# Kernel optimization log

Measured on AMD Instinct MI355X. Metric: run time of the kernel, lower is better.

Reference implementation:

```python
import jax, jax.numpy as jnp
import numpy as np

HEADS = 16
DIM_HEAD = 64

def setup_inputs() -> dict:
    key = jax.random.key(0)
    k1, k2, k3 = jax.random.split(key, 3)
    B, F, N, DIM = 4, 16, 196, 1024
    ntok = 1 + F * N  # cls + frames*patches
    x = jax.random.normal(k1, (B, ntok, DIM), dtype=jnp.float32)
    w_qkv = jax.random.normal(k2, (DIM, 3 * HEADS * DIM_HEAD), dtype=jnp.float32) * (DIM ** -0.5)
    w_out = jax.random.normal(k3, (HEADS * DIM_HEAD, DIM), dtype=jnp.float32) * ((HEADS * DIM_HEAD) ** -0.5)
    return {"x": x, "w_qkv": w_qkv, "w_out": w_out, "f": F}

def _attn(q, k, v):
    # q: [b, i, d], k/v: [b, j, d]
    sim = jnp.einsum('bid,bjd->bij', q, k)
    a = jax.nn.softmax(sim, axis=-1)
    return jnp.einsum('bij,bjd->bid', a, v)

def reference(x, w_qkv, w_out, f):
    B, ntok, dim = x.shape
    h, dh = HEADS, DIM_HEAD
    n = (ntok - 1) // f  # patches per frame
    scale = dh ** -0.5

    qkv = x @ w_qkv  # [B, ntok, 3*h*dh]
    q, k, v = jnp.split(qkv, 3, axis=-1)
    # 'b n (h d) -> (b h) n d'
    def split_heads(t):
        return t.reshape(B, ntok, h, dh).transpose(0, 2, 1, 3).reshape(B * h, ntok, dh)
    q, k, v = split_heads(q) * scale, split_heads(k), split_heads(v)

    cls_q, q_ = q[:, :1], q[:, 1:]
    cls_k, k_ = k[:, :1], k[:, 1:]
    cls_v, v_ = v[:, :1], v[:, 1:]

    # cls token attends to everything
    cls_out = _attn(cls_q, k, v)  # [(b h), 1, d]

    # axial rearrange: '(b h) (f n) d -> (b h f) n d' (spatial attention)
    def to_axial(t):
        return t.reshape(B * h, f, n, dh).reshape(B * h * f, n, dh)
    q_, k_, v_ = map(to_axial, (q_, k_, v_))

    # broadcast cls kv to each frame: 'b () d -> (b r) () d', r = f
    cls_k_r = jnp.repeat(cls_k, f, axis=0)
    cls_v_r = jnp.repeat(cls_v, f, axis=0)
    k_ = jnp.concatenate((cls_k_r, k_), axis=1)  # [(b h f), 1+n, d]
    v_ = jnp.concatenate((cls_v_r, v_), axis=1)

    out = _attn(q_, k_, v_)  # [(b h f), n, d]
    # back: '(b h f) n d -> (b h) (f n) d'
    out = out.reshape(B * h, f * n, dh)
    out = jnp.concatenate((cls_out, out), axis=1)  # [(b h), ntok, d]
    # '(b h) n d -> b n (h d)'
    out = out.reshape(B, h, ntok, dh).transpose(0, 2, 1, 3).reshape(B, ntok, h * dh)
    return out @ w_out
```

## Files before the change

kernel.cpp:

```cpp
#include <hip/hip_runtime.h>
#include <stdint.h>

typedef unsigned short u16;
typedef unsigned int u32;
typedef __attribute__((ext_vector_type(4))) float f32x4;
typedef __attribute__((ext_vector_type(4))) float float4v;
typedef __attribute__((ext_vector_type(8))) short short8;
typedef __attribute__((ext_vector_type(4))) u32 u32x4;
typedef __attribute__((ext_vector_type(4))) u16 u16x4;
typedef __attribute__((ext_vector_type(8))) u16 u16x8;

#define DEV static __device__ __forceinline__

#define NTOK 3137
#define MROWS 12548
#define NHEAD 16
#define DH 64
#define NKT 16

DEV float bf2f(u16 h){ u32 u = ((u32)h)<<16; float f; __builtin_memcpy(&f,&u,4); return f; }
DEV u16 f2bf(float f){ u32 u; __builtin_memcpy(&u,&f,4); u32 r = u + 0x7FFFu + ((u>>16)&1u); return (u16)(r>>16); }

DEV void gl_lds16(const u16* g, u16* l){
  __builtin_amdgcn_global_load_lds((const __attribute__((address_space(1))) void*)g,
                                   (__attribute__((address_space(3))) void*)l, 16, 0, 0);
}

#define BARRIER()  asm volatile("s_barrier" ::: "memory")
#define WAIT_LGKM0() asm volatile("s_waitcnt lgkmcnt(0)" ::: "memory")
#define WAIT_VM(n)  asm volatile("s_waitcnt vmcnt(" #n ")" ::: "memory")

__global__ __launch_bounds__(256) void cast_bf16_kernel(const float* __restrict__ in,
                                                        u16* __restrict__ out, int n4){
  int i = blockIdx.x*256 + threadIdx.x;
  int stride = gridDim.x*256;
  for(; i < n4; i += stride){
    float4v v = *(const float4v*)(in + (size_t)i*4);
    u16x4 o;
    for(int e=0;e<4;++e) o[e] = f2bf(v[e]);
    *(u16x4*)(out + (size_t)i*4) = o;
  }
}

__global__ void transpose_cast_kernel(const float* __restrict__ in, u16* __restrict__ out,
                                      int R, int C){
  __shared__ float tile[32][33];
  int c0 = blockIdx.x<<5, r0 = blockIdx.y<<5;
  int tx = threadIdx.x, ty = threadIdx.y;
  for(int k=0;k<32;k+=8) tile[ty+k][tx] = in[(size_t)(r0+ty+k)*C + c0+tx];
  __syncthreads();
  for(int k=0;k<32;k+=8) out[(size_t)(c0+ty+k)*R + r0+tx] = f2bf(tile[tx][ty+k]);
}

template<int EPI>
__global__ __launch_bounds__(512, 2) void gemm256_kernel(
    const u16* __restrict__ A, const u16* __restrict__ Bt,
    u16* __restrict__ Qb, u16* __restrict__ Kb, u16* __restrict__ Vb,
    float* __restrict__ Out, int Mtot, int tilesx)
{
  __shared__ __align__(16) char smem[131072];
  const int tid = threadIdx.x, lane = tid & 63, wid = tid >> 6;
  const int wr = wid >> 2, wc = wid & 3;

  const int nwg = gridDim.x, chunk = nwg >> 3, orig = blockIdx.x;
  const int wg = (orig & 7)*chunk + (orig >> 3);
  const int by = wg / tilesx, bx = wg - by*tilesx;
  const int m0 = by << 8, n0 = bx << 8;

  f32x4 acc[8][4];
  #pragma unroll
  for(int i=0;i<8;++i)
    #pragma unroll
    for(int j=0;j<4;++j) acc[i][j] = (f32x4){0.f,0.f,0.f,0.f};

  auto STAGE = [&](int t, int hi){
    const int bsel = t & 1;
    char* base = smem + bsel*65536 + ((hi>>1)<<15) + ((hi&1)<<14);
    const u16* mat = (hi < 2) ? A : Bt;
    const int rbase = ((hi < 2) ? m0 : n0) + ((hi&1)<<7);
    #pragma unroll
    for(int j=0;j<2;++j){
      int idx = j*512 + tid;
      int r = idx >> 3;
      int c2s = ((idx&7)<<4) ^ ((r&7)<<4);
      int grow = rbase + r;
      if(hi < 2 && grow >= Mtot) grow = Mtot - 1;
      const u16* src = mat + (size_t)grow*1024 + t*64 + (c2s>>1);
      u16* dst = (u16*)(base + j*8192 + wid*1024);
      gl_lds16(src, dst);
    }
  };

  const int rA   = (lane&15)*128;
  const int csw0 = (((lane>>4)<<4)      ) ^ ((lane&7)<<4);
  const int csw1 = (((lane>>4)<<4) + 64 ) ^ ((lane&7)<<4);

  auto RDA = [&](int bsel, int i, int kk)->short8 {
    const char* p = smem + bsel*65536 + (wr<<14) + (i<<4)*128 + rA + (kk ? csw1 : csw0);
    return *(const short8*)p;
  };
  auto RDB = [&](int bsel, int jn, int kk)->short8 {
    const char* p = smem + bsel*65536 + 32768 + ((wc>>1)<<14)
                  + (((wc&1)<<6) + (jn<<4))*128 + rA + (kk ? csw1 : csw0);
    return *(const short8*)p;
  };

  STAGE(0,0); STAGE(0,1); STAGE(0,2); STAGE(0,3); STAGE(1,0);
  WAIT_VM(2);
  BARRIER();

  short8 aR[4][2], b0[2][2], b1[2][2];
  for(int t=0; t<NKT; ++t){
    const int bs = t & 1;
    #pragma unroll
    for(int i=0;i<4;++i){ aR[i][0]=RDA(bs,i,0); aR[i][1]=RDA(bs,i,1); }
    #pragma unroll
    for(int j=0;j<2;++j){ b0[j][0]=RDB(bs,j,0); b0[j][1]=RDB(bs,j,1); }
    if(t+1<NKT) STAGE(t+1,1);
    BARRIER(); WAIT_LGKM0();
    __builtin_amdgcn_s_setprio(1);
    #pragma unroll
    for(int i=0;i<4;++i)
      #pragma unroll
      for(int j=0;j<2;++j){
        acc[i][j] = __builtin_amdgcn_mfma_f32_16x16x32_bf16(aR[i][0], b0[j][0], acc[i][j], 0,0,0);
        acc[i][j] = __builtin_amdgcn_mfma_f32_16x16x32_bf16(aR[i][1], b0[j][1], acc[i][j], 0,0,0);
      }
    __builtin_amdgcn_s_setprio(0);
    BARRIER();
    #pragma unroll
    for(int j=0;j<2;++j){ b1[j][0]=RDB(bs,2+j,0); b1[j][1]=RDB(bs,2+j,1); }
    if(t+1<NKT) STAGE(t+1,2);
    BARRIER(); WAIT_LGKM0();
    __builtin_amdgcn_s_setprio(1);
    #pragma unroll
    for(int i=0;i<4;++i)
      #pragma unroll
      for(int j=0;j<2;++j){
        acc[i][2+j] = __builtin_amdgcn_mfma_f32_16x16x32_bf16(aR[i][0], b1[j][0], acc[i][2+j], 0,0,0);
        acc[i][2+j] = __builtin_amdgcn_mfma_f32_16x16x32_bf16(aR[i][1], b1[j][1], acc[i][2+j], 0,0,0);
      }
    __builtin_amdgcn_s_setprio(0);
    BARRIER();
    #pragma unroll
    for(int i=0;i<4;++i){ aR[i][0]=RDA(bs,4+i,0); aR[i][1]=RDA(bs,4+i,1); }
    if(t+1<NKT) STAGE(t+1,3);
    BARRIER(); WAIT_LGKM0();
    __builtin_amdgcn_s_setprio(1);
    #pragma unroll
    for(int i=0;i<4;++i)
      #pragma unroll
      for(int j=0;j<2;++j){
        acc[4+i][2+j] = __builtin_amdgcn_mfma_f32_16x16x32_bf16(aR[i][0], b1[j][0], acc[4+i][2+j], 0,0,0);
        acc[4+i][2+j] = __builtin_amdgcn_mfma_f32_16x16x32_bf16(aR[i][1], b1[j][1], acc[4+i][2+j], 0,0,0);
      }
    __builtin_amdgcn_s_setprio(0);
    BARRIER();
    if(t+2<NKT) STAGE(t+2,0);
    if(t < NKT-2){ WAIT_VM(2); } else { WAIT_VM(0); }
    BARRIER();
    __builtin_amdgcn_s_setprio(1);
    #pragma unroll
    for(int i=0;i<4;++i)
      #pragma unroll
      for(int j=0;j<2;++j){
        acc[4+i][j] = __builtin_amdgcn_mfma_f32_16x16x32_bf16(aR[i][0], b0[j][0], acc[4+i][j], 0,0,0);
        acc[4+i][j] = __builtin_amdgcn_mfma_f32_16x16x32_bf16(aR[i][1], b0[j][1], acc[4+i][j], 0,0,0);
      }
    __builtin_amdgcn_s_setprio(0);
    BARRIER();
  }

  __syncthreads();

  if constexpr(EPI==0){
    const int which = n0 >> 10;
    const int hbase = (n0 & 1023) >> 6;
    const float sc = (which==0) ? 0.125f : 1.0f;
    u16* dst = (which==0)?Qb:((which==1)?Kb:Vb);
    u16* lC = (u16*)smem;
    for(int rh=0; rh<2; ++rh){
      if(wr == rh){
        #pragma unroll
        for(int i=0;i<8;++i){
          int rr = (i<<4) + ((lane>>4)<<2);
          #pragma unroll
          for(int j=0;j<4;++j){
            int ct = (wc<<6) + (j<<4) + (lane&15);
            #pragma unroll
            for(int r=0;r<4;++r) lC[(rr+r)*264 + ct] = f2bf(acc[i][j][r]*sc);
          }
        }
      }
      __syncthreads();
      for(int it=0; it<8; ++it){
        int idx = it*512 + tid;
        int row = idx >> 5, rest = idx & 31, hh = rest>>3, slot = rest&7;
        int mm = m0 + rh*128 + row;
        if(mm < Mtot){
          int b = mm / NTOK, tok = mm - b*NTOK;
          u16x8 v = *(const u16x8*)&lC[row*264 + hh*64 + slot*8];
          *(u16x8*)(dst + (((size_t)(b*NHEAD + hbase + hh)*NTOK + tok)<<6) + slot*8) = v;
        }
      }
      __syncthreads();
    }
  } else {
    float* lF = (float*)smem;
    for(int ph=0; ph<4; ++ph){
      int rh = ph>>1, ch = ph&1;
      if(wr==rh && (wc>>1)==ch){
        #pragma unroll
        for(int i=0;i<8;++i){
          int rr = (i<<4) + ((lane>>4)<<2);
          #pragma unroll
          for(int j=0;j<4;++j){
            int ct = ((wc&1)<<6) + (j<<4) + (lane&15);
            #pragma unroll
            for(int r=0;r<4;++r) lF[(rr+r)*132 + ct] = acc[i][j][r];
          }
        }
      }
      __syncthreads();
      for(int it=0; it<8; ++it){
        int idx = it*512 + tid;
        int row = idx >> 5, slot = idx & 31;
        int mm = m0 + rh*128 + row;
        if(mm < Mtot){
          float4v v = *(const float4v*)&lF[row*132 + slot*4];
          *(float4v*)(Out + (size_t)mm*1024 + n0 + ch*128 + slot*4) = v;
        }
      }
      __syncthreads();
    }
  }
}

__global__ __launch_bounds__(256) void cls_partial_kernel(
    const u16* __restrict__ Qb, const u16* __restrict__ Kb, const u16* __restrict__ Vb,
    float* __restrict__ part)
{
  __shared__ float qs[64];
  __shared__ float pbuf[4][64];
  __shared__ float wm[4], wl[4];
  __shared__ float wacc[4][64];
  const int tid = threadIdx.x, lane = tid & 63, wv = tid >> 6;
  const int c = blockIdx.x, bh = blockIdx.y;
  const u16* Kh = Kb + (size_t)bh*NTOK*DH;
  const u16* Vh = Vb + (size_t)bh*NTOK*DH;
  if(tid < 64) qs[tid] = bf2f(Qb[(size_t)bh*NTOK*DH + tid]);
  __syncthreads();

  const int jb = c*256 + wv*64;
  const int j = jb + lane;
  float s = -1e30f;
  if(j < NTOK){
    const u16* kr = Kh + (size_t)j*DH;
    float dot = 0.f;
    for(int t=0;t<8;++t){
      u16x8 kv = *(const u16x8*)(kr + t*8);
      for(int e=0;e<8;++e) dot += bf2f(kv[e]) * qs[t*8+e];
    }
    s = dot;
  }
  float mw = s;
  for(int off=1; off<64; off<<=1) mw = fmaxf(mw, __shfl_xor(mw, off));
  float p = (j < NTOK) ? __expf(s - mw) : 0.f;
  float lw = p;
  for(int off=1; off<64; off<<=1) lw += __shfl_xor(lw, off);
  pbuf[wv][lane] = p;

  float accd = 0.f;
  if(jb < NTOK){
    int nv = NTOK - jb; if(nv > 64) nv = 64;
    for(int jj=0; jj<nv; ++jj)
      accd += pbuf[wv][jj] * bf2f(Vh[(size_t)(jb+jj)*DH + lane]);
  }
  wacc[wv][lane] = accd;
  if(lane==0){ wm[wv]=mw; wl[wv]=lw; }
  __syncthreads();
  if(wv==0){
    float M = fmaxf(fmaxf(wm[0],wm[1]), fmaxf(wm[2],wm[3]));
    float L=0.f, Acc=0.f;
    for(int wi=0; wi<4; ++wi){
      float e = __expf(wm[wi]-M);
      L += wl[wi]*e; Acc += wacc[wi][lane]*e;
    }
    float* dstp = part + ((size_t)bh*13 + c)*68;
    if(lane==0){ dstp[0]=M; dstp[1]=L; }
    dstp[2+lane] = Acc;
  }
}

__global__ __launch_bounds__(64) void cls_reduce_kernel(
    const float* __restrict__ part, u16* __restrict__ Abuf)
{
  const int lane = threadIdx.x, bh = blockIdx.x;
  const float* p0 = part + (size_t)bh*13*68;
  float M = -1e30f;
  for(int i=0;i<13;++i) M = fmaxf(M, p0[i*68]);
  float L=0.f, Acc=0.f;
  for(int i=0;i<13;++i){
    float e = __expf(p0[i*68] - M);
    L += p0[i*68+1]*e;
    Acc += p0[i*68+2+lane]*e;
  }
  int b = bh>>4, h = bh&15;
  Abuf[(size_t)b*NTOK*1024 + h*DH + lane] = f2bf(Acc/L);
}

__global__ __launch_bounds__(256) void axial_attn_kernel(
    const u16* __restrict__ Qb, const u16* __restrict__ Kb, const u16* __restrict__ Vb,
    u16* __restrict__ Abuf)
{
  __shared__ u16 lV[64*232];
  __shared__ u16 lP[4*16*232];
  const int tid = threadIdx.x, lane = tid & 63, wv = tid >> 6;
  const int bf = blockIdx.x, bh = bf >> 4, fi = bf & 15;
  const u16* Kh = Kb + (size_t)bh*NTOK*DH;
  const u16* Vh = Vb + (size_t)bh*NTOK*DH;
  const u16* Qh = Qb + (size_t)bh*NTOK*DH;

  for(int c = tid; c < 224*8; c += 256){
    int tok = c >> 3, slot = c & 7;
    u16 vals[8];
    if(tok <= 196){
      size_t row = (tok==0) ? 0 : (size_t)(fi*196 + tok)*DH;
      u16x8 v = *(const u16x8*)(Vh + row + slot*8);
      for(int e=0;e<8;++e) vals[e] = v[e];
    } else {
      for(int e=0;e<8;++e) vals[e] = 0;
    }
    for(int e=0;e<8;++e) lV[(slot*8+e)*232 + tok] = vals[e];
  }
  for(int c = tid; c < 4*16*16; c += 256){
    int w2 = c >> 8, rem = c & 255, row = rem >> 4, cc = rem & 15;
    lP[w2*(16*232) + row*232 + 208 + cc] = 0;
  }
  __syncthreads();

  u16* myP = lP + wv*(16*232);
  const int b_i = bh >> 4, h = bh & 15;

  for(int qt = wv; qt < 13; qt += 4){
    int qr = qt*16 + (lane&15);
    int qrc = qr < 196 ? qr : 195;
    size_t qrow = (size_t)(1 + fi*196 + qrc)*DH;
    short8 qa0 = *(const short8*)(Qh + qrow + ((lane>>4)<<3));
    short8 qa1 = *(const short8*)(Qh + qrow + 32 + ((lane>>4)<<3));

    f32x4 s[13];
    for(int t=0;t<13;++t){
      int tok = t*16 + (lane&15);
      int tokc = tok < 197 ? tok : 196;
      size_t krow = (tokc==0) ? 0 : (size_t)(fi*196 + tokc)*DH;
      short8 b0v = *(const short8*)(Kh + krow + ((lane>>4)<<3));
      short8 b1v = *(const short8*)(Kh + krow + 32 + ((lane>>4)<<3));
      f32x4 z = {0.f,0.f,0.f,0.f};
      z = __builtin_amdgcn_mfma_f32_16x16x32_bf16(qa0, b0v, z, 0,0,0);
      z = __builtin_amdgcn_mfma_f32_16x16x32_bf16(qa1, b1v, z, 0,0,0);
      s[t] = z;
    }
    int mycol = lane & 15;
    if(192 + mycol >= 197)
      for(int r=0;r<4;++r) s[12][r] = -1e30f;

    f32x4 mx = s[0];
    for(int t=1;t<13;++t) for(int r=0;r<4;++r) mx[r] = fmaxf(mx[r], s[t][r]);
    for(int off=1; off<16; off<<=1)
      for(int r=0;r<4;++r) mx[r] = fmaxf(mx[r], __shfl_xor(mx[r], off));
    f32x4 lsum = {0.f,0.f,0.f,0.f};
    for(int t=0;t<13;++t) for(int r=0;r<4;++r){
      float p = __expf(s[t][r] - mx[r]); s[t][r] = p; lsum[r] += p;
    }
    for(int off=1; off<16; off<<=1)
      for(int r=0;r<4;++r) lsum[r] += __shfl_xor(lsum[r], off);

    for(int t=0;t<13;++t){
      int tok = t*16 + mycol;
      for(int r=0;r<4;++r) myP[(((lane>>4)<<2)+r)*232 + tok] = f2bf(s[t][r]);
    }

    f32x4 o[4] = {{0.f,0.f,0.f,0.f},{0.f,0.f,0.f,0.f},{0.f,0.f,0.f,0.f},{0.f,0.f,0.f,0.f}};
    for(int t2=0;t2<7;++t2){
      short8 a = *(const short8*)&myP[(lane&15)*232 + t2*32 + ((lane>>4)<<3)];
      for(int nd=0;nd<4;++nd){
        short8 b = *(const short8*)&lV[(nd*16 + (lane&15))*232 + t2*32 + ((lane>>4)<<3)];
        o[nd] = __builtin_amdgcn_mfma_f32_16x16x32_bf16(a, b, o[nd], 0,0,0);
      }
    }

    for(int nd=0; nd<4; ++nd){
      int d = nd*16 + (lane&15);
      for(int r=0;r<4;++r){
        int rr = ((lane>>4)<<2) + r;
        myP[rr*72 + d] = f2bf(o[nd][r] / lsum[r]);
      }
    }
    asm volatile("s_waitcnt lgkmcnt(0)" ::: "memory");
    for(int it=0; it<2; ++it){
      int idx = it*64 + lane;
      int row = idx >> 3, slot = idx & 7;
      int ql = qt*16 + row;
      if(ql < 196){
        u16x8 v = *(const u16x8*)&myP[row*72 + slot*8];
        int tok = 1 + fi*196 + ql;
        *(u16x8*)(Abuf + ((size_t)b_i*NTOK + tok)*1024 + h*DH + slot*8) = v;
      }
    }
  }
}

extern "C" void kernel_launch(void* const* d_in, const int* in_sizes, int n_in,
                              void* d_out, int out_size, void* d_ws, size_t ws_size,
                              hipStream_t stream) {
  const float* x     = (const float*)d_in[0];
  const float* wqkv  = (const float*)d_in[1];
  const float* wout  = (const float*)d_in[2];
  float* out = (float*)d_out;
  char* ws = (char*)d_ws;

  u16* xb     = (u16*)(ws);
  u16* Abuf   = xb;
  u16* wqkvT  = (u16*)(ws + 25698304);
  float* clsPart = (float*)(ws + 25698304);
  u16* woutT  = (u16*)(ws + 31989760);
  u16* Qb     = (u16*)(ws + 34086912);
  u16* Kb     = (u16*)(ws + 59785216);
  u16* Vb     = (u16*)(ws + 85483520);

  cast_bf16_kernel<<<dim3(2048), dim3(256), 0, stream>>>(x, xb, (MROWS*1024)/4);
  transpose_cast_kernel<<<dim3(96,32), dim3(32,8), 0, stream>>>(wqkv, wqkvT, 1024, 3072);
  transpose_cast_kernel<<<dim3(32,32), dim3(32,8), 0, stream>>>(wout, woutT, 1024, 1024);

  gemm256_kernel<0><<<dim3(600), dim3(512), 0, stream>>>(xb, wqkvT, Qb, Kb, Vb, nullptr, MROWS, 12);

  cls_partial_kernel<<<dim3(13,64), dim3(256), 0, stream>>>(Qb, Kb, Vb, clsPart);
  cls_reduce_kernel<<<dim3(64), dim3(64), 0, stream>>>(clsPart, Abuf);
  axial_attn_kernel<<<dim3(1024), dim3(256), 0, stream>>>(Qb, Kb, Vb, Abuf);

  gemm256_kernel<1><<<dim3(200), dim3(512), 0, stream>>>(Abuf, woutT, nullptr, nullptr, nullptr, out, MROWS, 4);
}
```

Before: 218.7 us.

## Deepen GEMM prefetch pipeline with reordered stage issue and relaxed waits

Restructures the QKV GEMM main loop to process two k-tiles per iteration and reorders which quarter-stages are prefetched at each step, so loads for tile t+2 are issued earlier. The vmcnt wait now sits after the last MFMA block of each tile instead of before it, allowing more outstanding global-to-LDS loads. A partial lgkmcnt wait is inserted before the first barrier. This aims to hide global load latency better, at the cost of more complex hazard reasoning on LDS buffer reuse.

```diff
diff --git a/kernel.cpp b/kernel.cpp
--- a/kernel.cpp
+++ b/kernel.cpp
@@ -105,70 +105,56 @@
     return *(const short8*)p;
   };
 
-  STAGE(0,0); STAGE(0,1); STAGE(0,2); STAGE(0,3); STAGE(1,0);
-  WAIT_VM(2);
-  BARRIER();
-
   short8 aR[4][2], b0[2][2], b1[2][2];
-  for(int t=0; t<NKT; ++t){
-    const int bs = t & 1;
-    #pragma unroll
-    for(int i=0;i<4;++i){ aR[i][0]=RDA(bs,i,0); aR[i][1]=RDA(bs,i,1); }
-    #pragma unroll
-    for(int j=0;j<2;++j){ b0[j][0]=RDB(bs,j,0); b0[j][1]=RDB(bs,j,1); }
-    if(t+1<NKT) STAGE(t+1,1);
-    BARRIER(); WAIT_LGKM0();
-    __builtin_amdgcn_s_setprio(1);
+
+  auto MFMA_Q = [&](int qi, int qj, short8 (&bv)[2][2]){
     #pragma unroll
     for(int i=0;i<4;++i)
       #pragma unroll
       for(int j=0;j<2;++j){
-        acc[i][j] = __builtin_amdgcn_mfma_f32_16x16x32_bf16(aR[i][0], b0[j][0], acc[i][j], 0,0,0);
-        acc[i][j] = __builtin_amdgcn_mfma_f32_16x16x32_bf16(aR[i][1], b0[j][1], acc[i][j], 0,0,0);
-      }
-    __builtin_amdgcn_s_setprio(0);
+        acc[qi*4+i][qj*2+j] = __builtin_amdgcn_mfma_f32_16x16x32_bf16(aR[i][0], bv[j][0], acc[qi*4+i][qj*2+j], 0,0,0);
+        acc[qi*4+i][qj*2+j] = __builtin_amdgcn_mfma_f32_16x16x32_bf16(aR[i][1], bv[j][1], acc[qi*4+i][qj*2+j], 0,0,0);
+      }
+  };
+
+  auto DO_TILE = [&](int bs, int st1,int sh1, int st2,int sh2, int st3,int sh3, int st4,int sh4, bool lastv){
+    #pragma unroll
+    for(int i=0;i<4;++i){ aR[i][0]=RDA(bs,i,0); aR[i][1]=RDA(bs,i,1); }
+    #pragma unroll
+    for(int j=0;j<2;++j){ b0[j][0]=RDB(bs,j,0); b0[j][1]=RDB(bs,j,1); }
+    if(st1 < NKT) STAGE(st1, sh1);
+    asm volatile("s_waitcnt lgkmcnt(8)" ::: "memory");
+    BARRIER(); WAIT_LGKM0();
+    __builtin_amdgcn_s_setprio(1); MFMA_Q(0,0,b0); __builtin_amdgcn_s_setprio(0);
     BARRIER();
     #pragma unroll
     for(int j=0;j<2;++j){ b1[j][0]=RDB(bs,2+j,0); b1[j][1]=RDB(bs,2+j,1); }
-    if(t+1<NKT) STAGE(t+1,2);
+    if(st2 < NKT) STAGE(st2, sh2);
     BARRIER(); WAIT_LGKM0();
-    __builtin_amdgcn_s_setprio(1);
-    #pragma unroll
-    for(int i=0;i<4;++i)
-      #pragma unroll
-      for(int j=0;j<2;++j){
-        acc[i][2+j] = __builtin_amdgcn_mfma_f32_16x16x32_bf16(aR[i][0], b1[j][0], acc[i][2+j], 0,0,0);
-        acc[i][2+j] = __builtin_amdgcn_mfma_f32_16x16x32_bf16(aR[i][1], b1[j][1], acc[i][2+j], 0,0,0);
-      }
-    __builtin_amdgcn_s_setprio(0);
+    __builtin_amdgcn_s_setprio(1); MFMA_Q(0,1,b1); __builtin_amdgcn_s_setprio(0);
     BARRIER();
     #pragma unroll
     for(int i=0;i<4;++i){ aR[i][0]=RDA(bs,4+i,0); aR[i][1]=RDA(bs,4+i,1); }
-    if(t+1<NKT) STAGE(t+1,3);
+    if(st3 < NKT) STAGE(st3, sh3);
     BARRIER(); WAIT_LGKM0();
-    __builtin_amdgcn_s_setprio(1);
-    #pragma unroll
-    for(int i=0;i<4;++i)
-      #pragma unroll
-      for(int j=0;j<2;++j){
-        acc[4+i][2+j] = __builtin_amdgcn_mfma_f32_16x16x32_bf16(aR[i][0], b1[j][0], acc[4+i][2+j], 0,0,0);
-        acc[4+i][2+j] = __builtin_amdgcn_mfma_f32_16x16x32_bf16(aR[i][1], b1[j][1], acc[4+i][2+j], 0,0,0);
-      }
-    __builtin_amdgcn_s_setprio(0);
+    __builtin_amdgcn_s_setprio(1); MFMA_Q(1,1,b1); __builtin_amdgcn_s_setprio(0);
     BARRIER();
-    if(t+2<NKT) STAGE(t+2,0);
-    if(t < NKT-2){ WAIT_VM(2); } else { WAIT_VM(0); }
+    if(st4 < NKT) STAGE(st4, sh4);
     BARRIER();
-    __builtin_amdgcn_s_setprio(1);
-    #pragma unroll
-    for(int i=0;i<4;++i)
-      #pragma unroll
-      for(int j=0;j<2;++j){
-        acc[4+i][j] = __builtin_amdgcn_mfma_f32_16x16x32_bf16(aR[i][0], b0[j][0], acc[4+i][j], 0,0,0);
-        acc[4+i][j] = __builtin_amdgcn_mfma_f32_16x16x32_bf16(aR[i][1], b0[j][1], acc[4+i][j], 0,0,0);
-      }
-    __builtin_amdgcn_s_setprio(0);
+    __builtin_amdgcn_s_setprio(1); MFMA_Q(1,0,b0); __builtin_amdgcn_s_setprio(0);
+    if(lastv){ WAIT_VM(0); } else { WAIT_VM(4); }
     BARRIER();
+  };
+
+  STAGE(0,2); STAGE(0,0); STAGE(0,3); STAGE(0,1); STAGE(1,2); STAGE(1,0);
+  WAIT_VM(4);
+  BARRIER();
+
+  for(int u=0; u<NKT/2; ++u){
+    const int tA = 2*u, tB = 2*u+1;
+    const bool last = (u == NKT/2-1);
+    DO_TILE(0, tB,3,   tB,1,   tA+2,2, tA+2,0, last);
+    DO_TILE(1, tA+2,3, tA+2,1, tB+2,2, tB+2,0, last);
   }
 
   __syncthreads();
```

Measured after the change: 212.8 us. 2.7% less time.
